# Kernel tuning notes

Hardware: AMD Instinct MI355X
Metric: run time of the kernel (lower is better)

Reference implementation:

```python
import jax, jax.numpy as jnp
import numpy as np

RWKV_K_CLAMP = 60.0
B, T, C = 8, 1024, 1024
LAYER_ID, N_LAYER = 2, 12


def _decay_speed():
    # replicate RWKV_TimeMix.__init__ decay_speed construction
    first = 1
    f1 = 3.0 + (LAYER_ID - first) / (N_LAYER - 1 - first) * (1.2 - 3.0)
    f2 = 0.65 + (LAYER_ID - first) / (N_LAYER - 1 - first) * (0.4 - 0.65)
    if LAYER_ID == first:
        f1 += 0.5
    if LAYER_ID == N_LAYER - 2:
        f2 = 0.4
    if LAYER_ID == N_LAYER - 1:
        f2 = 0.37
    h = np.arange(C, dtype=np.float64)
    return (f2 ** (h / (C - 1) * 7.0)) * f1


def setup_inputs() -> dict:
    key = jax.random.key(0)
    ks = jax.random.split(key, 6)
    scale = 1.0 / np.sqrt(C)
    time_mix = np.ones((C,), np.float32)
    time_mix[: C // 2] = 0.0
    return {
        "x": jax.random.normal(ks[0], (B, T, C), jnp.float32),
        "time_decay": jnp.asarray(np.log(_decay_speed()), jnp.float32),  # (C,)
        "time_first": jnp.full((C,), np.log(0.3), jnp.float32),
        "time_mix": jnp.asarray(time_mix),
        "combined_mix": jnp.full((C,), 0.01, jnp.float32),
        "Wk": jax.random.normal(ks[1], (C, C), jnp.float32) * scale,
        "Wv": jax.random.normal(ks[2], (C, C), jnp.float32) * scale,
        "Wr": jax.random.normal(ks[3], (C, C), jnp.float32) * scale,
        "Wo": jax.random.normal(ks[4], (C, C), jnp.float32) * scale,
    }


def _wkv(w, u, k, v):
    # w,u: (C,); k,v: (B,T,C). Numerically-stable decayed linear recurrence
    # (RWKV wkv kernel: running-max, like online softmax).
    b = k.shape[0]
    init = (
        jnp.zeros((b, C), k.dtype),            # numerator state a
        jnp.zeros((b, C), k.dtype),            # denominator state b
        jnp.full((b, C), -1e38, k.dtype),      # running max exponent p
    )

    def step(carry, kv):
        a, bb, p = carry
        kt, vt = kv  # (B,C)
        no = jnp.maximum(p, u + kt)
        e1 = jnp.exp(p - no)
        e2 = jnp.exp(u + kt - no)
        y = (e1 * a + e2 * vt) / (e1 * bb + e2)
        no2 = jnp.maximum(w + p, kt)
        e1 = jnp.exp(w + p - no2)
        e2 = jnp.exp(kt - no2)
        return (e1 * a + e2 * vt, e1 * bb + e2, no2), y

    _, y = jax.lax.scan(step, init, (k.transpose(1, 0, 2), v.transpose(1, 0, 2)))
    return y.transpose(1, 0, 2)  # (B,T,C)


def reference(x, time_decay, time_first, time_mix, combined_mix, Wk, Wv, Wr, Wo):
    b, t, c = x.shape
    zrow = jnp.zeros((b, 1, c), x.dtype)
    x_m1 = jnp.concatenate([zrow, x[:, :-1, :]], axis=1)   # time_shift / x_{t-1}
    x_p1 = jnp.concatenate([x[:, 1:, :], zrow], axis=1)    # x_{t+1}
    half = c // 2
    x_comb = jnp.concatenate([x_m1[:, :, :half], x_p1[:, :, half:]], axis=-1)
    xm = x * time_mix + x_m1 * (1.0 - time_mix) + x_comb * combined_mix
    k = jnp.exp(jnp.minimum(jnp.einsum("btc,dc->btd", xm, Wk), RWKV_K_CLAMP))
    v = jnp.einsum("btc,dc->btd", xm, Wv)
    r = jnp.einsum("btc,dc->btd", xm, Wr)
    wkv = _wkv(time_decay / t, time_first / t, k, v)
    return jnp.einsum("btc,dc->btd", jax.nn.sigmoid(r) * wkv, Wo)
```

## Files before the change

kernel.cpp:

```cpp
#include <hip/hip_runtime.h>
#include <hip/hip_bf16.h>
#include <stdint.h>

#define B_SZ 8
#define T_LEN 1024
#define C_DIM 1024
#define M_ROWS (B_SZ * T_LEN)
#define NCH 32
#define CHL (T_LEN / NCH)

typedef unsigned short ushort_t;
typedef __attribute__((ext_vector_type(8))) short short8;
typedef __attribute__((ext_vector_type(4))) float f32x4;
typedef __attribute__((ext_vector_type(4))) unsigned short us4;

static __device__ __forceinline__ float bf2f(ushort_t u) {
  union { unsigned int i; float f; } x; x.i = ((unsigned int)u) << 16; return x.f;
}
static __device__ __forceinline__ ushort_t f2bf(float f) {
  union { float f; unsigned int i; } x; x.f = f;
  unsigned int r = x.i + 0x7fffu + ((x.i >> 16) & 1u);
  return (ushort_t)(r >> 16);
}

static __device__ __forceinline__ void gload_lds16(const void* g, void* l) {
  __builtin_amdgcn_global_load_lds(
      (const __attribute__((address_space(1))) void*)g,
      (__attribute__((address_space(3))) void*)l, 16, 0, 0);
}

__global__ void prep_kernel(const float* __restrict__ wk, const float* __restrict__ wv,
                            const float* __restrict__ wr, const float* __restrict__ wo,
                            ushort_t* __restrict__ wob,
                            ushort_t* __restrict__ wf,
                            const float* __restrict__ x, const float* __restrict__ tm,
                            const float* __restrict__ cm, ushort_t* __restrict__ xmb) {
  const int bid = blockIdx.x;
  if (bid < 1024) {
    int gid = bid * 256 + threadIdx.x;
    float4 v = *(const float4*)(wo + (size_t)gid * 4);
    us4 o = {f2bf(v.x), f2bf(v.y), f2bf(v.z), f2bf(v.w)};
    *(us4*)(wob + (size_t)gid * 4) = o;
  } else if (bid < 2560) {
    int g = (bid - 1024) * 256 + threadIdx.x;
    int mode = g >> 17;
    int rem = g & 131071;
    int nf = rem >> 11;
    int rem2 = rem & 2047;
    int kt = rem2 >> 6;
    int l = rem2 & 63;
    const float* src = mode == 0 ? wk : mode == 1 ? wv : wr;
    const float* sp = src + (size_t)(nf * 16 + (l & 15)) * C_DIM + kt * 32 + (l >> 4) * 8;
    float4 v0 = *(const float4*)sp;
    float4 v1 = *(const float4*)(sp + 4);
    us4 o0 = {f2bf(v0.x), f2bf(v0.y), f2bf(v0.z), f2bf(v0.w)};
    us4 o1 = {f2bf(v1.x), f2bf(v1.y), f2bf(v1.z), f2bf(v1.w)};
    ushort_t* dst = wf + (size_t)g * 8;
    *(us4*)dst = o0;
    *(us4*)(dst + 4) = o1;
  } else {
    int gid = (bid - 2560) * 256 + threadIdx.x;
    int c4 = (gid & (C_DIM / 4 - 1)) * 4;
    int t = (gid >> 8) & (T_LEN - 1);
    const float4 zero = {0.f, 0.f, 0.f, 0.f};
    float4 xv = *(const float4*)(x + (size_t)gid * 4);
    float4 xp = (t > 0) ? *(const float4*)(x + (size_t)gid * 4 - C_DIM) : zero;
    float4 xn = (t < T_LEN - 1) ? *(const float4*)(x + (size_t)gid * 4 + C_DIM) : zero;
    float4 tmv = *(const float4*)(tm + c4);
    float4 cmv = *(const float4*)(cm + c4);
    float4 xc = (c4 < C_DIM / 2) ? xp : xn;
    us4 o;
    o.x = f2bf(xv.x * tmv.x + xp.x * (1.f - tmv.x) + xc.x * cmv.x);
    o.y = f2bf(xv.y * tmv.y + xp.y * (1.f - tmv.y) + xc.y * cmv.y);
    o.z = f2bf(xv.z * tmv.z + xp.z * (1.f - tmv.z) + xc.z * cmv.z);
    o.w = f2bf(xv.w * tmv.w + xp.w * (1.f - tmv.w) + xc.w * cmv.w);
    *(us4*)(xmb + (size_t)gid * 4) = o;
  }
}

__global__ __launch_bounds__(256, 4) void gemm_fused(const ushort_t* __restrict__ A,
                                                     const ushort_t* __restrict__ Wf,
                                                     ushort_t* __restrict__ outK,
                                                     ushort_t* __restrict__ outV,
                                                     ushort_t* __restrict__ outR) {
  constexpr int K = 1024;
  __shared__ ushort_t As[3][128 * 32];

  const int tid = threadIdx.x;
  const int lane = tid & 63;
  const int wave = tid >> 6;

  const int bid = blockIdx.x;
  const int xcd = bid & 7;
  const int r = bid >> 3;
  const int bm = (xcd * 8 + (r & 7)) * 128;
  const int jb = r >> 3;
  const int mode = jb >> 3;
  const int bn = (jb & 7) * 128;

  const int wr = (wave >> 1) * 64;
  const int wc = (wave & 1) * 64;

  f32x4 acc[4][4];
#pragma unroll
  for (int m = 0; m < 4; ++m)
#pragma unroll
    for (int n = 0; n < 4; ++n) acc[m][n] = (f32x4){0.f, 0.f, 0.f, 0.f};

  const int srow = tid >> 2;
  const int scol = (((tid & 3) ^ ((srow >> 1) & 3)) * 8);
  const ushort_t* Ag = A + (size_t)(bm + srow) * K + scol;

  const int fr = lane & 15;
  const int kq = lane >> 4;
  const int ps = (kq ^ ((fr >> 1) & 3)) * 8;

  const ushort_t* Bgl = Wf + ((size_t)mode << 20) +
                        (size_t)((jb & 7) * 8 + (wave & 1) * 4) * 16384 + lane * 8;

  auto stageA = [&](int buf, int kt) {
    const int k0 = kt * 32;
    ushort_t* ap = &As[buf][tid * 8];
    gload_lds16(Ag + k0, ap);
    gload_lds16(Ag + (size_t)64 * K + k0, ap + 64 * 32);
  };

  short8 b0[4], b1[4];

#define LOADB(DST, KT)                                                        \
  {                                                                           \
    _Pragma("unroll") for (int n = 0; n < 4; ++n)                             \
        DST[n] = *(const short8*)(Bgl + n * 16384 + (KT)*512);                \
  }

#define MFMA_STEP(ABUF, BREG)                                                 \
  {                                                                           \
    short8 af[4];                                                             \
    _Pragma("unroll") for (int m = 0; m < 4; ++m)                             \
        af[m] = *(const short8*)&As[ABUF][(wr + m * 16 + fr) * 32 + ps];      \
    _Pragma("unroll") for (int m = 0; m < 4; ++m)                             \
        _Pragma("unroll") for (int n = 0; n < 4; ++n)                         \
            acc[m][n] = __builtin_amdgcn_mfma_f32_16x16x32_bf16(              \
                af[m], BREG[n], acc[m][n], 0, 0, 0);                          \
  }

#define ENDSTEP(N)                                                            \
  asm volatile("s_waitcnt vmcnt(" #N ")" ::: "memory");                       \
  __builtin_amdgcn_s_barrier();                                               \
  __builtin_amdgcn_sched_barrier(0);

#define BODY(ACUR, ASTG, BCUR, BNXT, T)                                       \
  LOADB(BNXT, (T) + 1);                                                       \
  MFMA_STEP(ACUR, BCUR);                                                      \
  stageA(ASTG, (T) + 2);                                                      \
  ENDSTEP(6)

  stageA(0, 0);
  LOADB(b0, 0);
  stageA(1, 1);
  ENDSTEP(2)

#pragma unroll 1
  for (int i = 0; i < 5; ++i) {
    const int t0 = 6 * i;
    BODY(0, 2, b0, b1, t0 + 0)
    BODY(1, 0, b1, b0, t0 + 1)
    BODY(2, 1, b0, b1, t0 + 2)
    BODY(0, 2, b1, b0, t0 + 3)
    BODY(1, 0, b0, b1, t0 + 4)
    BODY(2, 1, b1, b0, t0 + 5)
  }
  LOADB(b1, 31);
  MFMA_STEP(0, b0);
  ENDSTEP(0)
  MFMA_STEP(1, b1);

#pragma unroll
  for (int m = 0; m < 4; ++m)
#pragma unroll
    for (int n = 0; n < 4; ++n)
#pragma unroll
      for (int j = 0; j < 4; ++j) {
        float v = acc[m][n][j];
        size_t idx = (size_t)(bm + wr + m * 16 + kq * 4 + j) * C_DIM + (bn + wc + n * 16 + fr);
        if (mode == 0) {
          outK[idx] = f2bf(__expf(fminf(v, 60.f)));
        } else if (mode == 1) {
          outV[idx] = f2bf(v);
        } else {
          outR[idx] = f2bf(1.f / (1.f + __expf(-v)));
        }
      }
#undef BODY
#undef ENDSTEP
#undef MFMA_STEP
#undef LOADB
}

__global__ __launch_bounds__(256, 2) void gemm_out(const ushort_t* __restrict__ A,
                                                   const ushort_t* __restrict__ Bw,
                                                   float* __restrict__ outF) {
  constexpr int K = 1024;
  constexpr int NT = K / 64;
  __shared__ ushort_t As[2][128 * 64];
  __shared__ ushort_t Bs[2][128 * 64];

  const int tid = threadIdx.x;
  const int l = tid & 63;
  const int wave = tid >> 6;
  const int fr = l & 15;
  const int kq = l >> 4;

  const int bid = blockIdx.x;
  const int xcd = bid & 7;
  const int idx = bid >> 3;
  const int jb = idx >> 3;
  const int bm = (xcd * 8 + (idx & 7)) * 128;
  const int bn = jb * 128;

  const int wr = (wave >> 1) * 64;
  const int wc = (wave & 1) * 64;

  f32x4 acc[4][4];
#pragma unroll
  for (int m = 0; m < 4; ++m)
#pragma unroll
    for (int n = 0; n < 4; ++n) acc[m][n] = (f32x4){0.f, 0.f, 0.f, 0.f};

  int srow[4], scol[4];
#pragma unroll
  for (int j = 0; j < 4; ++j) {
    int row = wave * 32 + j * 8 + (l >> 3);
    srow[j] = row;
    scol[j] = ((l & 7) ^ (row & 7)) * 8;
  }
  const ushort_t* AgB = A + (size_t)bm * K;
  const ushort_t* BgB = Bw + (size_t)bn * K;
  const int dst0 = wave * 2048 + l * 8;

  auto stage = [&](int buf, int k0) {
#pragma unroll
    for (int j = 0; j < 4; ++j)
      gload_lds16(AgB + (size_t)srow[j] * K + scol[j] + k0, &As[buf][dst0 + j * 512]);
#pragma unroll
    for (int j = 0; j < 4; ++j)
      gload_lds16(BgB + (size_t)srow[j] * K + scol[j] + k0, &Bs[buf][dst0 + j * 512]);
  };

  stage(0, 0);
  asm volatile("s_waitcnt vmcnt(0)" ::: "memory");
  __syncthreads();

  const int ps0 = ((0 * 4 + kq) ^ (fr & 7)) * 8;
  const int ps1 = ((1 * 4 + kq) ^ (fr & 7)) * 8;

  int cur = 0;
  for (int t = 0; t < NT; ++t) {
    if (t < NT - 1) stage(cur ^ 1, (t + 1) * 64);
    short8 af[4][2], bfr[4][2];
#pragma unroll
    for (int m = 0; m < 4; ++m) {
      af[m][0] = *(const short8*)&As[cur][(wr + m * 16 + fr) * 64 + ps0];
      af[m][1] = *(const short8*)&As[cur][(wr + m * 16 + fr) * 64 + ps1];
    }
#pragma unroll
    for (int n = 0; n < 4; ++n) {
      bfr[n][0] = *(const short8*)&Bs[cur][(wc + n * 16 + fr) * 64 + ps0];
      bfr[n][1] = *(const short8*)&Bs[cur][(wc + n * 16 + fr) * 64 + ps1];
    }
#pragma unroll
    for (int m = 0; m < 4; ++m)
#pragma unroll
      for (int n = 0; n < 4; ++n)
#pragma unroll
        for (int ks = 0; ks < 2; ++ks)
          acc[m][n] = __builtin_amdgcn_mfma_f32_16x16x32_bf16(af[m][ks], bfr[n][ks], acc[m][n], 0, 0, 0);
    asm volatile("s_waitcnt vmcnt(0)" ::: "memory");
    __syncthreads();
    cur ^= 1;
  }

#pragma unroll
  for (int m = 0; m < 4; ++m)
#pragma unroll
    for (int n = 0; n < 4; ++n)
#pragma unroll
      for (int j = 0; j < 4; ++j)
        outF[(size_t)(bm + wr + m * 16 + kq * 4 + j) * C_DIM + (bn + wc + n * 16 + fr)] =
            acc[m][n][j];
}

__global__ void wkv_phaseA(const ushort_t* __restrict__ kk, const ushort_t* __restrict__ vv,
                           const float* __restrict__ td,
                           float* __restrict__ sa, float* __restrict__ sb,
                           float* __restrict__ sp) {
  int gid = blockIdx.x * 256 + threadIdx.x;
  int c = gid & (C_DIM - 1);
  int ch = (gid >> 10) & (NCH - 1);
  int b = gid >> 15;
  float w = td[c] * (1.f / T_LEN);
  size_t base = ((size_t)b * T_LEN + ch * CHL) * C_DIM + c;
  float a = 0.f, bb = 0.f, p = -1e38f;
  for (int t = 0; t < CHL; ++t) {
    float kt = bf2f(kk[base + (size_t)t * C_DIM]);
    float vt = bf2f(vv[base + (size_t)t * C_DIM]);
    float no2 = fmaxf(w + p, kt);
    float e1 = __expf(w + p - no2);
    float e2 = __expf(kt - no2);
    a = e1 * a + e2 * vt;
    bb = e1 * bb + e2;
    p = no2;
  }
  sa[gid] = a; sb[gid] = bb; sp[gid] = p;
}

__global__ void wkv_phaseC2(const ushort_t* __restrict__ kk, const ushort_t* __restrict__ vv,
                            const ushort_t* __restrict__ sr, const float* __restrict__ td,
                            const float* __restrict__ tf,
                            const float* __restrict__ sa, const float* __restrict__ sb,
                            const float* __restrict__ sp, ushort_t* __restrict__ sy) {
  int gid = blockIdx.x * 256 + threadIdx.x;
  int c = gid & (C_DIM - 1);
  int ch = (gid >> 10) & (NCH - 1);
  int b = gid >> 15;
  float w = td[c] * (1.f / T_LEN);
  float u = tf[c] * (1.f / T_LEN);
  float wL = w * (float)CHL;

  float a = 0.f, bb = 0.f, p = -1e38f;
  size_t sbase = ((size_t)b * NCH) * C_DIM + c;
  for (int j = 0; j < ch; ++j) {
    float ac = sa[sbase + (size_t)j * C_DIM];
    float bc = sb[sbase + (size_t)j * C_DIM];
    float pc = sp[sbase + (size_t)j * C_DIM];
    float pn = fmaxf(p + wL, pc);
    float e1 = __expf(p + wL - pn);
    float e2 = __expf(pc - pn);
    a = e1 * a + e2 * ac;
    bb = e1 * bb + e2 * bc;
    p = pn;
  }

  size_t base = ((size_t)b * T_LEN + ch * CHL) * C_DIM + c;
  for (int t = 0; t < CHL; ++t) {
    float kt = bf2f(kk[base + (size_t)t * C_DIM]);
    float vt = bf2f(vv[base + (size_t)t * C_DIM]);
    float no = fmaxf(p, u + kt);
    float e1 = __expf(p - no);
    float e2 = __expf(u + kt - no);
    float y = (e1 * a + e2 * vt) / (e1 * bb + e2);
    float srv = bf2f(sr[base + (size_t)t * C_DIM]);
    sy[base + (size_t)t * C_DIM] = f2bf(srv * y);
    float no2 = fmaxf(w + p, kt);
    e1 = __expf(w + p - no2);
    e2 = __expf(kt - no2);
    a = e1 * a + e2 * vt;
    bb = e1 * bb + e2;
    p = no2;
  }
}

extern "C" void kernel_launch(void* const* d_in, const int* in_sizes, int n_in,
                              void* d_out, int out_size, void* d_ws, size_t ws_size,
                              hipStream_t stream) {
  const float* x  = (const float*)d_in[0];
  const float* td = (const float*)d_in[1];
  const float* tf = (const float*)d_in[2];
  const float* tm = (const float*)d_in[3];
  const float* cm = (const float*)d_in[4];
  const float* Wk = (const float*)d_in[5];
  const float* Wv = (const float*)d_in[6];
  const float* Wr = (const float*)d_in[7];
  const float* Wo = (const float*)d_in[8];

  const size_t MC = (size_t)M_ROWS * C_DIM;
  const size_t CC = (size_t)C_DIM * C_DIM;

  char* ws = (char*)d_ws;
  ushort_t* xmb = (ushort_t*)ws; ws += MC * 2;
  ushort_t* Wob = (ushort_t*)ws; ws += CC * 2;
  ushort_t* Wfr = (ushort_t*)ws; ws += 3 * CC * 2;
  ushort_t* kk  = (ushort_t*)ws; ws += MC * 2;
  ushort_t* vv  = (ushort_t*)ws; ws += MC * 2;
  ushort_t* sr  = (ushort_t*)ws; ws += MC * 2;
  ushort_t* sy  = (ushort_t*)ws; ws += MC * 2;
  float* sa = (float*)ws; ws += (size_t)B_SZ * NCH * C_DIM * 4;
  float* sb = (float*)ws; ws += (size_t)B_SZ * NCH * C_DIM * 4;
  float* sp = (float*)ws; ws += (size_t)B_SZ * NCH * C_DIM * 4;

  prep_kernel<<<dim3(10752), 256, 0, stream>>>(Wk, Wv, Wr, Wo, Wob, Wfr, x, tm, cm, xmb);

  gemm_fused<<<dim3(1536), 256, 0, stream>>>(xmb, Wfr, kk, vv, sr);

  wkv_phaseA<<<(B_SZ * NCH * C_DIM) / 256, 256, 0, stream>>>(kk, vv, td, sa, sb, sp);
  wkv_phaseC2<<<(B_SZ * NCH * C_DIM) / 256, 256, 0, stream>>>(kk, vv, sr, td, tf, sa, sb, sp, sy);

  gemm_out<<<dim3(512), 256, 0, stream>>>(sy, Wob, (float*)d_out);
}
```

Before: 149.0 us.

## Unify GEMMs into templated 256x128-tile kernel with register-fed pre-fragmented weights

```diff
diff --git a/kernel.cpp b/kernel.cpp
--- a/kernel.cpp
+++ b/kernel.cpp
@@ -31,25 +31,19 @@
 
 __global__ void prep_kernel(const float* __restrict__ wk, const float* __restrict__ wv,
                             const float* __restrict__ wr, const float* __restrict__ wo,
-                            ushort_t* __restrict__ wob,
                             ushort_t* __restrict__ wf,
                             const float* __restrict__ x, const float* __restrict__ tm,
                             const float* __restrict__ cm, ushort_t* __restrict__ xmb) {
   const int bid = blockIdx.x;
-  if (bid < 1024) {
-    int gid = bid * 256 + threadIdx.x;
-    float4 v = *(const float4*)(wo + (size_t)gid * 4);
-    us4 o = {f2bf(v.x), f2bf(v.y), f2bf(v.z), f2bf(v.w)};
-    *(us4*)(wob + (size_t)gid * 4) = o;
-  } else if (bid < 2560) {
-    int g = (bid - 1024) * 256 + threadIdx.x;
+  if (bid < 2048) {
+    int g = bid * 256 + threadIdx.x;
     int mode = g >> 17;
     int rem = g & 131071;
     int nf = rem >> 11;
     int rem2 = rem & 2047;
     int kt = rem2 >> 6;
     int l = rem2 & 63;
-    const float* src = mode == 0 ? wk : mode == 1 ? wv : wr;
+    const float* src = mode == 0 ? wk : mode == 1 ? wv : mode == 2 ? wr : wo;
     const float* sp = src + (size_t)(nf * 16 + (l & 15)) * C_DIM + kt * 32 + (l >> 4) * 8;
     float4 v0 = *(const float4*)sp;
     float4 v1 = *(const float4*)(sp + 4);
@@ -59,7 +53,7 @@
     *(us4*)dst = o0;
     *(us4*)(dst + 4) = o1;
   } else {
-    int gid = (bid - 2560) * 256 + threadIdx.x;
+    int gid = (bid - 2048) * 256 + threadIdx.x;
     int c4 = (gid & (C_DIM / 4 - 1)) * 4;
     int t = (gid >> 8) & (T_LEN - 1);
     const float4 zero = {0.f, 0.f, 0.f, 0.f};
@@ -78,28 +72,32 @@
   }
 }
 
-__global__ __launch_bounds__(256, 4) void gemm_fused(const ushort_t* __restrict__ A,
-                                                     const ushort_t* __restrict__ Wf,
-                                                     ushort_t* __restrict__ outK,
-                                                     ushort_t* __restrict__ outV,
-                                                     ushort_t* __restrict__ outR) {
+template <int FUSED>
+__global__ __launch_bounds__(512, 4) void gemm_main(const ushort_t* __restrict__ A,
+                                                    const ushort_t* __restrict__ Wf,
+                                                    float* __restrict__ outF,
+                                                    ushort_t* __restrict__ outK,
+                                                    ushort_t* __restrict__ outV,
+                                                    ushort_t* __restrict__ outR) {
   constexpr int K = 1024;
-  __shared__ ushort_t As[3][128 * 32];
+  __shared__ ushort_t As[3][256 * 32];
 
   const int tid = threadIdx.x;
   const int lane = tid & 63;
-  const int wave = tid >> 6;
+  const int wid = tid >> 6;
+  const int wm = wid & 3;
+  const int wn = wid >> 2;
 
   const int bid = blockIdx.x;
   const int xcd = bid & 7;
-  const int r = bid >> 3;
-  const int bm = (xcd * 8 + (r & 7)) * 128;
-  const int jb = r >> 3;
-  const int mode = jb >> 3;
-  const int bn = (jb & 7) * 128;
-
-  const int wr = (wave >> 1) * 64;
-  const int wc = (wave & 1) * 64;
+  const int c = bid >> 3;
+  const int bm = (xcd * 4 + (c & 3)) * 256;
+  const int jb = c >> 2;
+  const int mode = FUSED ? (jb >> 3) : 3;
+  const int bn = FUSED ? (jb & 7) * 128 : jb * 128;
+
+  const int wr = wm * 64;
+  const int wc = wn * 64;
 
   f32x4 acc[4][4];
 #pragma unroll
@@ -107,22 +105,23 @@
 #pragma unroll
     for (int n = 0; n < 4; ++n) acc[m][n] = (f32x4){0.f, 0.f, 0.f, 0.f};
 
-  const int srow = tid >> 2;
-  const int scol = (((tid & 3) ^ ((srow >> 1) & 3)) * 8);
-  const ushort_t* Ag = A + (size_t)(bm + srow) * K + scol;
+  const int a0r = tid >> 2, a0c = (((tid & 3) ^ ((tid >> 3) & 3)) * 8);
+  const int c1 = tid + 512;
+  const int a1r = c1 >> 2, a1c = (((c1 & 3) ^ ((c1 >> 3) & 3)) * 8);
+  const ushort_t* Ag0 = A + (size_t)(bm + a0r) * K + a0c;
+  const ushort_t* Ag1 = A + (size_t)(bm + a1r) * K + a1c;
 
   const int fr = lane & 15;
   const int kq = lane >> 4;
   const int ps = (kq ^ ((fr >> 1) & 3)) * 8;
 
-  const ushort_t* Bgl = Wf + ((size_t)mode << 20) +
-                        (size_t)((jb & 7) * 8 + (wave & 1) * 4) * 16384 + lane * 8;
+  const int nfbase = (bn >> 4) + wn * 4;
+  const ushort_t* Bgl = Wf + ((size_t)mode << 20) + (size_t)nfbase * 16384 + lane * 8;
 
   auto stageA = [&](int buf, int kt) {
     const int k0 = kt * 32;
-    ushort_t* ap = &As[buf][tid * 8];
-    gload_lds16(Ag + k0, ap);
-    gload_lds16(Ag + (size_t)64 * K + k0, ap + 64 * 32);
+    gload_lds16(Ag0 + k0, &As[buf][tid * 8]);
+    gload_lds16(Ag1 + k0, &As[buf][(tid + 512) * 8]);
   };
 
   short8 b0[4], b1[4];
@@ -187,107 +186,16 @@
           outK[idx] = f2bf(__expf(fminf(v, 60.f)));
         } else if (mode == 1) {
           outV[idx] = f2bf(v);
+        } else if (mode == 2) {
+          outR[idx] = f2bf(1.f / (1.f + __expf(-v)));
         } else {
-          outR[idx] = f2bf(1.f / (1.f + __expf(-v)));
+          outF[idx] = v;
         }
       }
 #undef BODY
 #undef ENDSTEP
 #undef MFMA_STEP
 #undef LOADB
-}
-
-__global__ __launch_bounds__(256, 2) void gemm_out(const ushort_t* __restrict__ A,
-                                                   const ushort_t* __restrict__ Bw,
-                                                   float* __restrict__ outF) {
-  constexpr int K = 1024;
-  constexpr int NT = K / 64;
-  __shared__ ushort_t As[2][128 * 64];
-  __shared__ ushort_t Bs[2][128 * 64];
-
-  const int tid = threadIdx.x;
-  const int l = tid & 63;
-  const int wave = tid >> 6;
-  const int fr = l & 15;
-  const int kq = l >> 4;
-
-  const int bid = blockIdx.x;
-  const int xcd = bid & 7;
-  const int idx = bid >> 3;
-  const int jb = idx >> 3;
-  const int bm = (xcd * 8 + (idx & 7)) * 128;
-  const int bn = jb * 128;
-
-  const int wr = (wave >> 1) * 64;
-  const int wc = (wave & 1) * 64;
-
-  f32x4 acc[4][4];
-#pragma unroll
-  for (int m = 0; m < 4; ++m)
-#pragma unroll
-    for (int n = 0; n < 4; ++n) acc[m][n] = (f32x4){0.f, 0.f, 0.f, 0.f};
-
-  int srow[4], scol[4];
-#pragma unroll
-  for (int j = 0; j < 4; ++j) {
-    int row = wave * 32 + j * 8 + (l >> 3);
-    srow[j] = row;
-    scol[j] = ((l & 7) ^ (row & 7)) * 8;
-  }
-  const ushort_t* AgB = A + (size_t)bm * K;
-  const ushort_t* BgB = Bw + (size_t)bn * K;
-  const int dst0 = wave * 2048 + l * 8;
-
-  auto stage = [&](int buf, int k0) {
-#pragma unroll
-    for (int j = 0; j < 4; ++j)
-      gload_lds16(AgB + (size_t)srow[j] * K + scol[j] + k0, &As[buf][dst0 + j * 512]);
-#pragma unroll
-    for (int j = 0; j < 4; ++j)
-      gload_lds16(BgB + (size_t)srow[j] * K + scol[j] + k0, &Bs[buf][dst0 + j * 512]);
-  };
-
-  stage(0, 0);
-  asm volatile("s_waitcnt vmcnt(0)" ::: "memory");
-  __syncthreads();
-
-  const int ps0 = ((0 * 4 + kq) ^ (fr & 7)) * 8;
-  const int ps1 = ((1 * 4 + kq) ^ (fr & 7)) * 8;
-
-  int cur = 0;
-  for (int t = 0; t < NT; ++t) {
-    if (t < NT - 1) stage(cur ^ 1, (t + 1) * 64);
-    short8 af[4][2], bfr[4][2];
-#pragma unroll
-    for (int m = 0; m < 4; ++m) {
-      af[m][0] = *(const short8*)&As[cur][(wr + m * 16 + fr) * 64 + ps0];
-      af[m][1] = *(const short8*)&As[cur][(wr + m * 16 + fr) * 64 + ps1];
-    }
-#pragma unroll
-    for (int n = 0; n < 4; ++n) {
-      bfr[n][0] = *(const short8*)&Bs[cur][(wc + n * 16 + fr) * 64 + ps0];
-      bfr[n][1] = *(const short8*)&Bs[cur][(wc + n * 16 + fr) * 64 + ps1];
-    }
-#pragma unroll
-    for (int m = 0; m < 4; ++m)
-#pragma unroll
-      for (int n = 0; n < 4; ++n)
-#pragma unroll
-        for (int ks = 0; ks < 2; ++ks)
-          acc[m][n] = __builtin_amdgcn_mfma_f32_16x16x32_bf16(af[m][ks], bfr[n][ks], acc[m][n], 0, 0, 0);
-    asm volatile("s_waitcnt vmcnt(0)" ::: "memory");
-    __syncthreads();
-    cur ^= 1;
-  }
-
-#pragma unroll
-  for (int m = 0; m < 4; ++m)
-#pragma unroll
-    for (int n = 0; n < 4; ++n)
-#pragma unroll
-      for (int j = 0; j < 4; ++j)
-        outF[(size_t)(bm + wr + m * 16 + kq * 4 + j) * C_DIM + (bn + wc + n * 16 + fr)] =
-            acc[m][n][j];
 }
 
 __global__ void wkv_phaseA(const ushort_t* __restrict__ kk, const ushort_t* __restrict__ vv,
@@ -378,8 +286,7 @@
 
   char* ws = (char*)d_ws;
   ushort_t* xmb = (ushort_t*)ws; ws += MC * 2;
-  ushort_t* Wob = (ushort_t*)ws; ws += CC * 2;
-  ushort_t* Wfr = (ushort_t*)ws; ws += 3 * CC * 2;
+  ushort_t* Wf  = (ushort_t*)ws; ws += 4 * CC * 2;
   ushort_t* kk  = (ushort_t*)ws; ws += MC * 2;
   ushort_t* vv  = (ushort_t*)ws; ws += MC * 2;
   ushort_t* sr  = (ushort_t*)ws; ws += MC * 2;
@@ -388,12 +295,12 @@
   float* sb = (float*)ws; ws += (size_t)B_SZ * NCH * C_DIM * 4;
   float* sp = (float*)ws; ws += (size_t)B_SZ * NCH * C_DIM * 4;
 
-  prep_kernel<<<dim3(10752), 256, 0, stream>>>(Wk, Wv, Wr, Wo, Wob, Wfr, x, tm, cm, xmb);
-
-  gemm_fused<<<dim3(1536), 256, 0, stream>>>(xmb, Wfr, kk, vv, sr);
+  prep_kernel<<<dim3(10240), 256, 0, stream>>>(Wk, Wv, Wr, Wo, Wf, x, tm, cm, xmb);
+
+  gemm_main<1><<<dim3(768), 512, 0, stream>>>(xmb, Wf, nullptr, kk, vv, sr);
 
   wkv_phaseA<<<(B_SZ * NCH * C_DIM) / 256, 256, 0, stream>>>(kk, vv, td, sa, sb, sp);
   wkv_phaseC2<<<(B_SZ * NCH * C_DIM) / 256, 256, 0, stream>>>(kk, vv, sr, td, tf, sa, sb, sp, sy);
 
-  gemm_out<<<dim3(512), 256, 0, stream>>>(sy, Wob, (float*)d_out);
-}
+  gemm_main<0><<<dim3(256), 512, 0, stream>>>(sy, Wf, (float*)d_out, nullptr, nullptr, nullptr);
+}
```

Result: slower. 160.0 us (+7.4%).
